# Kernel tuning notes

Measured on AMD Instinct MI355X. Metric: run time of the kernel, lower is better.

The kernel has to match this reference:

```python
import jax, jax.numpy as jnp
import numpy as np

D_MODEL = 2048
N_HEADS = 32
N_KV = 8
HEAD_DIM = D_MODEL // N_HEADS  # 64
D_FF = 8192
ROPE_BASE = 10000.0
EPS = 1e-5
B, S = 2, 2048


def setup_inputs() -> dict:
    key = jax.random.key(0)
    ks = jax.random.split(key, 8)
    s = 0.02
    qkv_out = (N_HEADS + 2 * N_KV) * HEAD_DIM
    return {
        "x": jax.random.normal(ks[0], (B, S, D_MODEL), jnp.float32),
        "w_norm1": jnp.ones((D_MODEL,), jnp.float32),
        "w_qkv": jax.random.normal(ks[1], (D_MODEL, qkv_out), jnp.float32) * s,
        "w_out": jax.random.normal(ks[2], (D_MODEL, D_MODEL), jnp.float32) * s,
        "w_norm2": jnp.ones((D_MODEL,), jnp.float32),
        "w_gate": jax.random.normal(ks[3], (D_MODEL, D_FF), jnp.float32) * s,
        "w_up": jax.random.normal(ks[4], (D_MODEL, D_FF), jnp.float32) * s,
        "w_down": jax.random.normal(ks[5], (D_FF, D_MODEL), jnp.float32) * s,
    }


def _rmsnorm(x, w):
    var = jnp.mean(x * x, axis=-1, keepdims=True)
    return x * jax.lax.rsqrt(var + EPS) * w


def _rope(x, cos, sin):
    # x: [b, s, h, d]; cos/sin: [s, d/2]; non-interleaved (NeoX half split)
    half = x.shape[-1] // 2
    x1, x2 = x[..., :half], x[..., half:]
    c = cos[None, :, None, :]
    sn = sin[None, :, None, :]
    return jnp.concatenate([x1 * c - x2 * sn, x1 * sn + x2 * c], axis=-1)


def _forward(x, w_norm1, w_qkv, w_out, w_norm2, w_gate, w_up, w_down):
    b, s, d = x.shape
    # --- attention block ---
    h = _rmsnorm(x, w_norm1)
    qkv = h @ w_qkv  # [b, s, (H + 2*KV) * hd]
    q = qkv[..., : N_HEADS * HEAD_DIM].reshape(b, s, N_HEADS, HEAD_DIM)
    kv = qkv[..., N_HEADS * HEAD_DIM:].reshape(b, s, 2, N_KV, HEAD_DIM)
    k, v = kv[:, :, 0], kv[:, :, 1]

    inv_freq = 1.0 / (ROPE_BASE ** (jnp.arange(0, HEAD_DIM, 2, dtype=jnp.float32) / HEAD_DIM))
    t = jnp.arange(s, dtype=jnp.float32)
    freqs = t[:, None] * inv_freq[None, :]  # [s, hd/2]
    cos, sin = jnp.cos(freqs), jnp.sin(freqs)
    q = _rope(q, cos, sin)
    k = _rope(k, cos, sin)

    # GQA: repeat_interleave kv heads to match q heads
    g = N_HEADS // N_KV
    k = jnp.repeat(k, g, axis=2)  # [b, s, H, hd]
    v = jnp.repeat(v, g, axis=2)

    scale = 1.0 / np.sqrt(HEAD_DIM)
    scores = jnp.einsum("bqhd,bkhd->bhqk", q, k) * scale
    causal = jnp.tril(jnp.ones((s, s), bool))
    scores = jnp.where(causal[None, None], scores, jnp.finfo(scores.dtype).min)
    attn = jax.nn.softmax(scores, axis=-1)
    ctx = jnp.einsum("bhqk,bkhd->bqhd", attn, v).reshape(b, s, N_HEADS * HEAD_DIM)
    x = x + ctx @ w_out

    # --- MLP block (SwiGLU) ---
    h2 = _rmsnorm(x, w_norm2)
    mlp = (jax.nn.silu(h2 @ w_gate) * (h2 @ w_up)) @ w_down
    return x + mlp


def reference(x, w_norm1, w_qkv, w_out, w_norm2, w_gate, w_up, w_down):
    return _forward(x, w_norm1, w_qkv, w_out, w_norm2, w_gate, w_up, w_down)
```

## Files before the change

kernel.cpp:

```cpp
#include <hip/hip_runtime.h>
#include <stdint.h>

#define D_MODEL 2048
#define S_LEN   2048
#define NTOK    4096
#define QKV_N   3072
#define DFF     8192

typedef float  f32x4   __attribute__((ext_vector_type(4)));
typedef float  f32x16  __attribute__((ext_vector_type(16)));
typedef __bf16 bf16x8  __attribute__((ext_vector_type(8)));
typedef unsigned short u16;
typedef unsigned short u16x8 __attribute__((ext_vector_type(8)));

__device__ __forceinline__ float b2f(u16 u){ union{float f; uint32_t i;} v; v.i = ((uint32_t)u) << 16; return v.f; }
__device__ __forceinline__ u16 f2b(float f){
  union{float f; uint32_t i;} v; v.f = f;
  uint32_t r = v.i + 0x7FFFu + ((v.i >> 16) & 1u);
  return (u16)(r >> 16);
}

__device__ __forceinline__ void gload_lds16(const void* gsrc, void* ldst){
  __builtin_amdgcn_global_load_lds(
      (const __attribute__((address_space(1))) void*)gsrc,
      (__attribute__((address_space(3))) void*)ldst,
      16, 0, 0);
}

__global__ __launch_bounds__(256) void wconv_kernel(const float* __restrict__ W, u16* __restrict__ WT,
                                                    int Nfull, int Kt, int Nt, int k0g, int n0g)
{
  __shared__ float tile[64][65];
  const int nTn = Nt >> 6;
  const int tk = blockIdx.x / nTn, tn = blockIdx.x % nTn;
  const int k0 = tk << 6, n0 = tn << 6;
  const int t  = threadIdx.x;
  const int c4 = (t & 15) << 2;
  const int r  = t >> 4;
#pragma unroll
  for (int i = 0; i < 4; ++i) {
    float4 v = *reinterpret_cast<const float4*>(&W[(size_t)(k0g + k0 + r + i*16) * Nfull + n0g + n0 + c4]);
    tile[r + i*16][c4+0] = v.x; tile[r + i*16][c4+1] = v.y;
    tile[r + i*16][c4+2] = v.z; tile[r + i*16][c4+3] = v.w;
  }
  __syncthreads();
#pragma unroll
  for (int i = 0; i < 4; ++i) {
    int n = r + i*16;
    ushort4 ov;
    ov.x = f2b(tile[c4+0][n]); ov.y = f2b(tile[c4+1][n]);
    ov.z = f2b(tile[c4+2][n]); ov.w = f2b(tile[c4+3][n]);
    *reinterpret_cast<ushort4*>(&WT[(size_t)(n0 + n) * Kt + k0 + c4]) = ov;
  }
}

__global__ void sincos_kernel(float* __restrict__ ct, float* __restrict__ st)
{
  int idx = blockIdx.x * 256 + threadIdx.x;
  if (idx >= S_LEN * 32) return;
  int p = idx >> 5, i = idx & 31;
  double freq = pow(10000.0, -((double)(2*i)) / 64.0);
  double ang  = (double)p * freq;
  ct[idx] = (float)cos(ang);
  st[idx] = (float)sin(ang);
}

template<bool BF16IN>
__global__ __launch_bounds__(256) void rmsnorm_kernel(const void* __restrict__ xin, const float* __restrict__ w, u16* __restrict__ out)
{
  const int row = blockIdx.x;
  const int t = threadIdx.x;
  float v[8];
  if (BF16IN) {
    const u16* xr = ((const u16*)xin) + (size_t)row * D_MODEL;
    u16x8 a = *reinterpret_cast<const u16x8*>(&xr[t*8]);
#pragma unroll
    for (int j = 0; j < 8; ++j) v[j] = b2f(a[j]);
  } else {
    const float* xr = ((const float*)xin) + (size_t)row * D_MODEL;
    float4 a = *reinterpret_cast<const float4*>(&xr[t*8]);
    float4 c = *reinterpret_cast<const float4*>(&xr[t*8+4]);
    v[0]=a.x; v[1]=a.y; v[2]=a.z; v[3]=a.w; v[4]=c.x; v[5]=c.y; v[6]=c.z; v[7]=c.w;
  }
  float ss = 0.f;
#pragma unroll
  for (int j = 0; j < 8; ++j) ss += v[j]*v[j];
#pragma unroll
  for (int d = 1; d < 64; d <<= 1) ss += __shfl_xor(ss, d);
  __shared__ float red[4];
  if ((t & 63) == 0) red[t >> 6] = ss;
  __syncthreads();
  ss = red[0] + red[1] + red[2] + red[3];
  const float sc = rsqrtf(ss * (1.0f / (float)D_MODEL) + 1e-5f);
  float4 w0 = *reinterpret_cast<const float4*>(&w[t*8]);
  float4 w1 = *reinterpret_cast<const float4*>(&w[t*8+4]);
  u16x8 o;
  o[0]=f2b(v[0]*sc*w0.x); o[1]=f2b(v[1]*sc*w0.y); o[2]=f2b(v[2]*sc*w0.z); o[3]=f2b(v[3]*sc*w0.w);
  o[4]=f2b(v[4]*sc*w1.x); o[5]=f2b(v[5]*sc*w1.y); o[6]=f2b(v[6]*sc*w1.z); o[7]=f2b(v[7]*sc*w1.w);
  *reinterpret_cast<u16x8*>(&out[(size_t)row * D_MODEL + t*8]) = o;
}

template<int EPI>
__device__ __forceinline__ void epi_store(size_t idx, float v, float* Cf, u16* Cb,
                                          const float* resf, const u16* resb, const u16* other)
{
  if (EPI == 2)      Cb[idx] = f2b(v / (1.0f + __expf(-v)));
  else if (EPI == 3) Cb[idx] = f2b(v * b2f(other[idx]));
  else if (EPI == 4) Cb[idx] = f2b(v);
  else if (EPI == 5) Cf[idx] += v;
  else if (EPI == 6) Cb[idx] = f2b(v + resf[idx]);
  else if (EPI == 7) Cf[idx] = v + b2f(resb[idx]);
}

template<int EPI>
__global__ __launch_bounds__(512, 2) void gemm8p_kernel(
    const u16* __restrict__ A, const u16* __restrict__ BT,
    int K, int lda, int ldb, int ldc, int n_off,
    float* Cf, u16* Cb,
    const float* __restrict__ resf, const u16* __restrict__ resb, const u16* other)
{
  __shared__ u16 lds[65536];
  const int tid = threadIdx.x;
  const int w = tid >> 6, lane = tid & 63;
  const int g = lane >> 4, lr = lane & 15;
  const int wm = w >> 2, wn = w & 3;
  const int bn = blockIdx.x, bm = blockIdx.y;
  const int NT = K >> 6;
  const int NI = NT >> 1;

  const int srow = tid >> 3;
  const int sg   = (tid & 7) ^ (srow & 7);
  const u16* Asrc = A  + (size_t)(bm * 256) * lda;
  const u16* Bsrc = BT + (size_t)(bn * 256) * ldb;

  const int agc0 = ((0 + g) ^ (lr & 7)) * 8;
  const int agc1 = ((4 + g) ^ (lr & 7)) * 8;

  f32x4 acc[8][4];
#pragma unroll
  for (int i = 0; i < 8; ++i)
#pragma unroll
    for (int j = 0; j < 4; ++j) acc[i][j] = (f32x4){0.f, 0.f, 0.f, 0.f};
  bf16x8 af[4][2], bf0[2][2], bf1[2][2];

#define STAGE_H(isB, h, b, T) do {                                           \
    int tc = ((T) < NT) ? (T) : (NT - 1);                                    \
    const u16* sb = (isB) ? Bsrc : Asrc;                                     \
    const int  sld = (isB) ? ldb : lda;                                      \
    const u16* s0 = sb + (size_t)((h)*128 + srow) * sld + tc*64 + sg*8;      \
    u16* dst = &lds[(b)*32768 + (isB)*16384 + (h)*8192 + tid*8];             \
    gload_lds16(s0, dst);                                                    \
    gload_lds16(s0 + (size_t)64 * sld, dst + 4096);                          \
  } while (0)

#define LOADA(mih, b) { _Pragma("unroll") for (int q = 0; q < 4; ++q) {      \
    const u16* rp = &lds[(b)*32768 + (wm*128 + (mih)*64 + q*16 + lr) * 64];  \
    af[q][0] = *(const bf16x8*)(rp + agc0);                                  \
    af[q][1] = *(const bf16x8*)(rp + agc1); } }

#define LOADB(dst, nih, b) { _Pragma("unroll") for (int nq = 0; nq < 2; ++nq) { \
    const u16* rp = &lds[(b)*32768 + 16384 + (wn*64 + (nih)*32 + nq*16 + lr) * 64]; \
    dst[nq][0] = *(const bf16x8*)(rp + agc0);                                \
    dst[nq][1] = *(const bf16x8*)(rp + agc1); } }

#define MM(mih, nih, BF) {                                                   \
    __builtin_amdgcn_s_setprio(1);                                           \
    _Pragma("unroll") for (int kk = 0; kk < 2; ++kk)                         \
      _Pragma("unroll") for (int q = 0; q < 4; ++q)                          \
        _Pragma("unroll") for (int nq = 0; nq < 2; ++nq)                     \
          acc[(mih)*4+q][(nih)*2+nq] = __builtin_amdgcn_mfma_f32_16x16x32_bf16( \
              af[q][kk], BF[nq][kk], acc[(mih)*4+q][(nih)*2+nq], 0, 0, 0);   \
    __builtin_amdgcn_s_setprio(0); }

#define SYNC_MID  __builtin_amdgcn_s_barrier();                              \
                  asm volatile("s_waitcnt lgkmcnt(0)" ::: "memory");         \
                  __builtin_amdgcn_sched_barrier(0);
#define PHEND     __builtin_amdgcn_s_barrier();
#define PHEND_VM  asm volatile("s_waitcnt vmcnt(4)" ::: "memory");           \
                  __builtin_amdgcn_s_barrier();

  STAGE_H(0, 0, 0, 0); STAGE_H(0, 1, 0, 0);
  STAGE_H(1, 0, 0, 0); STAGE_H(1, 1, 0, 0);
  STAGE_H(1, 0, 1, 1); STAGE_H(1, 1, 1, 1);
  asm volatile("s_waitcnt vmcnt(4)" ::: "memory");
  __builtin_amdgcn_s_barrier();

  for (int i = 0; i < NI; ++i) {
    const int t0 = 2 * i;
    LOADA(0, 0); LOADB(bf0, 0, 0);
    STAGE_H(0, 0, 1, t0 + 1);
    SYNC_MID; MM(0, 0, bf0); PHEND;
    LOADB(bf1, 1, 0);
    STAGE_H(0, 1, 1, t0 + 1);
    SYNC_MID; MM(0, 1, bf1); PHEND;
    LOADA(1, 0);
    STAGE_H(1, 0, 0, t0 + 2);
    SYNC_MID; MM(1, 1, bf1); PHEND;
    STAGE_H(1, 1, 0, t0 + 2);
    SYNC_MID; MM(1, 0, bf0); PHEND_VM;
    LOADA(0, 1); LOADB(bf0, 0, 1);
    STAGE_H(0, 0, 0, t0 + 2);
    SYNC_MID; MM(0, 0, bf0); PHEND;
    LOADB(bf1, 1, 1);
    STAGE_H(0, 1, 0, t0 + 2);
    SYNC_MID; MM(0, 1, bf1); PHEND;
    LOADA(1, 1);
    STAGE_H(1, 0, 1, t0 + 3);
    SYNC_MID; MM(1, 1, bf1); PHEND;
    STAGE_H(1, 1, 1, t0 + 3);
    SYNC_MID; MM(1, 0, bf0); PHEND_VM;
  }
#undef STAGE_H
#undef LOADA
#undef LOADB
#undef MM

#pragma unroll
  for (int mi = 0; mi < 8; ++mi) {
    const int rowOff = (mi >> 2) * 64 + (mi & 3) * 16;
#pragma unroll
    for (int ni = 0; ni < 4; ++ni) {
      const int colOff = (ni >> 1) * 32 + (ni & 1) * 16;
#pragma unroll
      for (int j = 0; j < 4; ++j) {
        int row = bm*256 + wm*128 + rowOff + g*4 + j;
        int col = n_off + bn*256 + wn*64 + colOff + lr;
        epi_store<EPI>((size_t)row * ldc + col, acc[mi][ni][j], Cf, Cb, resf, resb, other);
      }
    }
  }
}

template<int EPI>
__global__ __launch_bounds__(512) void gemm128_kernel(
    const u16* __restrict__ A, const u16* __restrict__ BT,
    int K, int lda, int ldb, int ldc, int n_off,
    float* Cf, u16* Cb,
    const float* __restrict__ resf, const u16* __restrict__ resb, const u16* other)
{
  __shared__ u16 lds[49152];
  const int tid = threadIdx.x;
  const int w = tid >> 6, lane = tid & 63;
  const int g = lane >> 4, lr = lane & 15;
  const int wm = w >> 2, wn = w & 3;
  const int bn = blockIdx.x, bm = blockIdx.y;
  const int NT = K >> 6;
  const int NI = NT >> 1;

  const int srow = tid >> 3;
  const int sg   = (tid & 7) ^ (srow & 7);
  const u16* Asrc = A  + (size_t)(bm * 128) * lda;
  const u16* Bsrc = BT + (size_t)(bn * 256) * ldb;

  const int agc0 = ((0 + g) ^ (lr & 7)) * 8;
  const int agc1 = ((4 + g) ^ (lr & 7)) * 8;

  f32x4 acc[4][4];
#pragma unroll
  for (int i = 0; i < 4; ++i)
#pragma unroll
    for (int j = 0; j < 4; ++j) acc[i][j] = (f32x4){0.f, 0.f, 0.f, 0.f};
  bf16x8 af[2][2], bf0[2][2], bf1[2][2];

#define STAGE_A(b, T) do {                                                   \
    int tc = ((T) < NT) ? (T) : (NT - 1);                                    \
    const u16* s0 = Asrc + (size_t)srow * lda + tc*64 + sg*8;                \
    u16* dst = &lds[(b)*24576 + tid*8];                                      \
    gload_lds16(s0, dst);                                                    \
    gload_lds16(s0 + (size_t)64 * lda, dst + 4096);                          \
  } while (0)

#define STAGE_BH(h, b, T) do {                                               \
    int tc = ((T) < NT) ? (T) : (NT - 1);                                    \
    const u16* s0 = Bsrc + (size_t)((h)*128 + srow) * ldb + tc*64 + sg*8;    \
    u16* dst = &lds[(b)*24576 + 8192 + (h)*8192 + tid*8];                    \
    gload_lds16(s0, dst);                                                    \
    gload_lds16(s0 + (size_t)64 * ldb, dst + 4096);                         \
  } while (0)

#define LOADA(mih, b) { _Pragma("unroll") for (int q = 0; q < 2; ++q) {      \
    const u16* rp = &lds[(b)*24576 + (wm*64 + (mih)*32 + q*16 + lr) * 64];   \
    af[q][0] = *(const bf16x8*)(rp + agc0);                                  \
    af[q][1] = *(const bf16x8*)(rp + agc1); } }

#define LOADB(dst, nih, b) { _Pragma("unroll") for (int nq = 0; nq < 2; ++nq) { \
    const u16* rp = &lds[(b)*24576 + 8192 + (wn*64 + (nih)*32 + nq*16 + lr) * 64]; \
    dst[nq][0] = *(const bf16x8*)(rp + agc0);                                \
    dst[nq][1] = *(const bf16x8*)(rp + agc1); } }

#define MM(mih, nih, BF) {                                                   \
    __builtin_amdgcn_s_setprio(1);                                           \
    _Pragma("unroll") for (int kk = 0; kk < 2; ++kk)                         \
      _Pragma("unroll") for (int q = 0; q < 2; ++q)                          \
        _Pragma("unroll") for (int nq = 0; nq < 2; ++nq)                     \
          acc[(mih)*2+q][(nih)*2+nq] = __builtin_amdgcn_mfma_f32_16x16x32_bf16( \
              af[q][kk], BF[nq][kk], acc[(mih)*2+q][(nih)*2+nq], 0, 0, 0);   \
    __builtin_amdgcn_s_setprio(0); }

  STAGE_A(0, 0); STAGE_BH(0, 0, 0); STAGE_BH(1, 0, 0);
  STAGE_BH(0, 1, 1); STAGE_BH(1, 1, 1);
  asm volatile("s_waitcnt vmcnt(4)" ::: "memory");
  __builtin_amdgcn_s_barrier();

  for (int i = 0; i < NI; ++i) {
    const int t0 = 2 * i;
    LOADA(0, 0); LOADB(bf0, 0, 0);
    STAGE_A(1, t0 + 1);
    SYNC_MID; MM(0, 0, bf0); PHEND;
    LOADB(bf1, 1, 0);
    STAGE_BH(0, 0, t0 + 2);
    SYNC_MID; MM(0, 1, bf1); PHEND;
    LOADA(1, 0);
    STAGE_BH(1, 0, t0 + 2);
    SYNC_MID; MM(1, 1, bf1); PHEND;
    STAGE_A(0, t0 + 2);
    SYNC_MID; MM(1, 0, bf0);
    asm volatile("s_waitcnt vmcnt(6)" ::: "memory");
    __builtin_amdgcn_s_barrier();
    LOADA(0, 1); LOADB(bf0, 0, 1);
    SYNC_MID; MM(0, 0, bf0); PHEND;
    LOADB(bf1, 1, 1);
    STAGE_BH(0, 1, t0 + 3);
    SYNC_MID; MM(0, 1, bf1); PHEND;
    LOADA(1, 1);
    STAGE_BH(1, 1, t0 + 3);
    SYNC_MID; MM(1, 1, bf1); PHEND;
    SYNC_MID; MM(1, 0, bf0);
    asm volatile("s_waitcnt vmcnt(4)" ::: "memory");
    __builtin_amdgcn_s_barrier();
  }
#undef STAGE_A
#undef STAGE_BH
#undef LOADA
#undef LOADB
#undef MM
#undef SYNC_MID
#undef PHEND
#undef PHEND_VM

#pragma unroll
  for (int mi = 0; mi < 4; ++mi) {
    const int rowOff = (mi >> 1) * 32 + (mi & 1) * 16;
#pragma unroll
    for (int ni = 0; ni < 4; ++ni) {
      const int colOff = (ni >> 1) * 32 + (ni & 1) * 16;
#pragma unroll
      for (int j = 0; j < 4; ++j) {
        int row = bm*128 + wm*64 + rowOff + g*4 + j;
        int col = n_off + bn*256 + wn*64 + colOff + lr;
        epi_store<EPI>((size_t)row * ldc + col, acc[mi][ni][j], Cf, Cb, resf, resb, other);
      }
    }
  }
}

__global__ __launch_bounds__(256) void rope_kernel(
    const u16* __restrict__ qkv, const float* __restrict__ ct, const float* __restrict__ st,
    u16* __restrict__ Q, u16* __restrict__ Kt, u16* __restrict__ VT)
{
  const int tok = blockIdx.x;
  const int b = tok >> 11, s = tok & (S_LEN - 1);
  const int w = threadIdx.x >> 6, lane = threadIdx.x & 63;
  const size_t base = (size_t)tok * QKV_N;
  for (int slot = w; slot < 48; slot += 4) {
    int col = (slot < 32) ? slot * 64 : (slot < 40 ? 2048 + (slot - 32) * 64 : 2560 + (slot - 40) * 64);
    float v = b2f(qkv[base + col + lane]);
    if (slot < 40) {
      int i = lane & 31;
      float c = ct[s * 32 + i], sn = st[s * 32 + i];
      float p = b2f(qkv[base + col + (lane ^ 32)]);
      v = (lane < 32) ? (v * c - p * sn) : (v * c + p * sn);
    }
    u16 ob = f2b(v);
    if (slot < 32)      Q [((size_t)(b * 32 + slot)      * S_LEN + s) * 64 + lane] = ob;
    else if (slot < 40) Kt[((size_t)(b * 8 + slot - 32)  * S_LEN + s) * 64 + lane] = ob;
    else                VT[((size_t)(b * 8 + slot - 40)  * 64 + lane) * S_LEN + s] = ob;
  }
}

#define ASCALE 0.1803368801111204f
__global__ __launch_bounds__(256, 3) void attn_kernel(
    const u16* __restrict__ Q, const u16* __restrict__ Kt,
    const u16* __restrict__ VT, u16* __restrict__ ctx)
{
  const int bh  = blockIdx.x;
  const int qb  = 15 - blockIdx.y;
  const int wid = threadIdx.x >> 6;
  const int lane = threadIdx.x & 63;
  const int b = bh >> 5, h = bh & 31;
  const int kvh = (b << 3) + (h >> 2);
  const int q0 = qb * 128 + wid * 32;
  const int cq = lane & 31;
  const int hi = lane >> 5;

  const u16* Qb = Q  + ((size_t)bh * S_LEN + q0) * 64;
  const u16* Kp = Kt + (size_t)kvh * S_LEN * 64 + cq * 64 + hi * 8;
  const u16* Vbase = VT + (size_t)kvh * 64 * S_LEN + hi * 8;
  const u16* Vp[4];
#pragma unroll
  for (int v = 0; v < 4; ++v)
    Vp[v] = Vbase + (size_t)((v & 1) * 32 + cq) * S_LEN + (v >> 1) * 16;

  bf16x8 qf[4];
#pragma unroll
  for (int t = 0; t < 4; ++t)
    qf[t] = *reinterpret_cast<const bf16x8*>(&Qb[cq * 64 + t * 16 + hi * 8]);

  f32x16 o0 = {}, o1 = {};
  float m = -1e30f, l = 0.f;

  __shared__ float xch[4][32];

  const int nt = qb * 4 + wid + 1;

#define ATT_LOADK(KF, T) { _Pragma("unroll") for (int q_ = 0; q_ < 4; ++q_) \
    KF[q_] = *(const bf16x8*)(Kp + (T) * 2048 + q_ * 16); }
#define ATT_LOADV(VF, T) { _Pragma("unroll") for (int v_ = 0; v_ < 4; ++v_) \
    VF[v_] = *(const bf16x8*)(Vp[v_] + (T) * 32); }

#define ATT_COMPUTE(KF, VF, T) do {                                          \
    f32x16 sA = {}, sB = {};                                                 \
    sA = __builtin_amdgcn_mfma_f32_32x32x16_bf16(KF[0], qf[0], sA, 0, 0, 0); \
    sB = __builtin_amdgcn_mfma_f32_32x32x16_bf16(KF[1], qf[1], sB, 0, 0, 0); \
    sA = __builtin_amdgcn_mfma_f32_32x32x16_bf16(KF[2], qf[2], sA, 0, 0, 0); \
    sB = __builtin_amdgcn_mfma_f32_32x32x16_bf16(KF[3], qf[3], sB, 0, 0, 0); \
    float p[16];                                                             \
    _Pragma("unroll") for (int r = 0; r < 16; ++r) p[r] = (sA[r] + sB[r]) * ASCALE; \
    if ((T) == nt - 1) {                                                     \
      _Pragma("unroll") for (int r = 0; r < 16; ++r) {                       \
        int kk = (r & 3) + 8 * (r >> 2) + 4 * hi;                            \
        if (kk > cq) p[r] = -1e30f;                                          \
      }                                                                      \
    }                                                                        \
    float m0_ = fmaxf(fmaxf(p[0], p[1]), p[2]);                              \
    float m1_ = fmaxf(fmaxf(p[3], p[4]), p[5]);                              \
    float m2_ = fmaxf(fmaxf(p[6], p[7]), p[8]);                              \
    float m3_ = fmaxf(fmaxf(p[9], p[10]), p[11]);                            \
    float m4_ = fmaxf(fmaxf(p[12], p[13]), p[14]);                           \
    float tmax = fmaxf(fmaxf(fmaxf(m0_, m1_), m2_), fmaxf(fmaxf(m3_, m4_), p[15])); \
    tmax = fmaxf(tmax, __shfl_xor(tmax, 32));                                \
    if (!__all(tmax <= m + 8.0f)) {                                          \
      float mn = fmaxf(m, tmax);                                             \
      float corr = exp2f(m - mn);                                            \
      m = mn;                                                                \
      l *= corr;                                                             \
      if (hi == 0) xch[wid][cq] = corr;                                      \
      asm volatile("s_waitcnt lgkmcnt(0)" ::: "memory");                     \
      __builtin_amdgcn_sched_barrier(0);                                     \
      float4 c0 = *reinterpret_cast<const float4*>(&xch[wid][4 * hi + 0]);   \
      float4 c1 = *reinterpret_cast<const float4*>(&xch[wid][4 * hi + 8]);   \
      float4 c2 = *reinterpret_cast<const float4*>(&xch[wid][4 * hi + 16]);  \
      float4 c3 = *reinterpret_cast<const float4*>(&xch[wid][4 * hi + 24]);  \
      float ca[16] = {c0.x,c0.y,c0.z,c0.w, c1.x,c1.y,c1.z,c1.w,              \
                      c2.x,c2.y,c2.z,c2.w, c3.x,c3.y,c3.z,c3.w};             \
      _Pragma("unroll") for (int r = 0; r < 16; ++r) { o0[r] *= ca[r]; o1[r] *= ca[r]; } \
    }                                                                        \
    float tsum = 0.f;                                                        \
    _Pragma("unroll") for (int r = 0; r < 16; ++r) { p[r] = exp2f(p[r] - m); tsum += p[r]; } \
    l += tsum;                                                               \
    uint32_t wds[8], pw[8];                                                  \
    _Pragma("unroll") for (int j = 0; j < 8; ++j) {                          \
      uint32_t wv;                                                           \
      asm("v_cvt_pk_bf16_f32 %0, %1, %2" : "=v"(wv) : "v"(p[2*j]), "v"(p[2*j+1])); \
      wds[j] = wv;                                                           \
    }                                                                        \
    _Pragma("unroll") for (int j = 0; j < 8; ++j) pw[j] = __shfl_xor(wds[j], 32); \
    union { uint32_t u[4]; bf16x8 v; } pa0, pa1;                             \
    pa0.u[0] = hi ? pw[2]  : wds[0];                                         \
    pa0.u[1] = hi ? pw[3]  : wds[1];                                         \
    pa0.u[2] = hi ? wds[2] : pw[0];                                          \
    pa0.u[3] = hi ? wds[3] : pw[1];                                          \
    pa1.u[0] = hi ? pw[6]  : wds[4];                                         \
    pa1.u[1] = hi ? pw[7]  : wds[5];                                         \
    pa1.u[2] = hi ? wds[6] : pw[4];                                          \
    pa1.u[3] = hi ? wds[7] : pw[5];                                          \
    o0 = __builtin_amdgcn_mfma_f32_32x32x16_bf16(pa0.v, VF[0], o0, 0, 0, 0); \
    o0 = __builtin_amdgcn_mfma_f32_32x32x16_bf16(pa1.v, VF[2], o0, 0, 0, 0); \
    o1 = __builtin_amdgcn_mfma_f32_32x32x16_bf16(pa0.v, VF[1], o1, 0, 0, 0); \
    o1 = __builtin_amdgcn_mfma_f32_32x32x16_bf16(pa1.v, VF[3], o1, 0, 0, 0); \
  } while (0)

  bf16x8 kf0[4], kf1[4], vf[4];
  ATT_LOADK(kf0, 0);
  for (int t = 0; t < nt; ) {
    if (t + 1 < nt) ATT_LOADK(kf1, t + 1);
    ATT_LOADV(vf, t);
    ATT_COMPUTE(kf0, vf, t);
    ++t; if (t >= nt) break;
    if (t + 1 < nt) ATT_LOADK(kf0, t + 1);
    ATT_LOADV(vf, t);
    ATT_COMPUTE(kf1, vf, t);
    ++t;
  }
#undef ATT_LOADK
#undef ATT_LOADV
#undef ATT_COMPUTE

  l += __shfl_xor(l, 32);
  float linv = 1.0f / l;
  if (hi == 0) xch[wid][cq] = linv;
  asm volatile("s_waitcnt lgkmcnt(0)" ::: "memory");
  __builtin_amdgcn_sched_barrier(0);
  float4 n0 = *reinterpret_cast<const float4*>(&xch[wid][4 * hi + 0]);
  float4 n1 = *reinterpret_cast<const float4*>(&xch[wid][4 * hi + 8]);
  float4 n2 = *reinterpret_cast<const float4*>(&xch[wid][4 * hi + 16]);
  float4 n3 = *reinterpret_cast<const float4*>(&xch[wid][4 * hi + 24]);
  float na[16] = {n0.x,n0.y,n0.z,n0.w, n1.x,n1.y,n1.z,n1.w,
                  n2.x,n2.y,n2.z,n2.w, n3.x,n3.y,n3.z,n3.w};
#pragma unroll
  for (int r = 0; r < 16; ++r) {
    int row = (r & 3) + 8 * (r >> 2) + 4 * hi;
    size_t base = (size_t)(b * S_LEN + q0 + row) * D_MODEL + h * 64;
    ctx[base + cq]      = f2b(o0[r] * na[r]);
    ctx[base + 32 + cq] = f2b(o1[r] * na[r]);
  }
}

extern "C" void kernel_launch(void* const* d_in, const int* in_sizes, int n_in,
                              void* d_out, int out_size, void* d_ws, size_t ws_size,
                              hipStream_t stream)
{
  const float* x     = (const float*)d_in[0];
  const float* wn1   = (const float*)d_in[1];
  const float* wqkv  = (const float*)d_in[2];
  const float* wout  = (const float*)d_in[3];
  const float* wn2   = (const float*)d_in[4];
  const float* wgate = (const float*)d_in[5];
  const float* wup   = (const float*)d_in[6];
  const float* wdown = (const float*)d_in[7];
  float* out = (float*)d_out;
  char* ws = (char*)d_ws;

  float* cosT = (float*)(ws + 0);
  float* sinT = (float*)(ws + 262144);
  u16*   wT   = (u16*)  (ws + 524288);
  u16*   hB   = (u16*)  (ws + 17301504);
  u16*   x1b  = (u16*)  (ws + 34078720);
  char*  S    = ws + 50855936;
  u16*   qkvB = (u16*)(S + 0);
  u16*   qB   = (u16*)(S + 25165824);
  u16*   kB   = (u16*)(S + 41943040);
  u16*   vtB  = (u16*)(S + 46137344);
  u16*   ctxB = (u16*)(S + 50331648);
  u16*   gsB  = (u16*)(S + 0);

  sincos_kernel<<<dim3(256), 256, 0, stream>>>(cosT, sinT);
  rmsnorm_kernel<false><<<dim3(NTOK), 256, 0, stream>>>(x, wn1, hB);

  wconv_kernel<<<dim3((2048/64)*(3072/64)), 256, 0, stream>>>(wqkv, wT, 3072, 2048, 3072, 0, 0);
  gemm128_kernel<4><<<dim3(QKV_N/256, NTOK/128), 512, 0, stream>>>(hB, wT, 2048, 2048, 2048, 3072, 0, nullptr, qkvB, nullptr, nullptr, nullptr);
  rope_kernel<<<dim3(NTOK), 256, 0, stream>>>(qkvB, cosT, sinT, qB, kB, vtB);
  attn_kernel<<<dim3(64, 16), 256, 0, stream>>>(qB, kB, vtB, ctxB);

  wconv_kernel<<<dim3((2048/64)*(2048/64)), 256, 0, stream>>>(wout, wT, 2048, 2048, 2048, 0, 0);
  gemm128_kernel<6><<<dim3(D_MODEL/256, NTOK/128), 512, 0, stream>>>(ctxB, wT, 2048, 2048, 2048, 2048, 0, nullptr, x1b, x, nullptr, nullptr);

  rmsnorm_kernel<true><<<dim3(NTOK), 256, 0, stream>>>(x1b, wn2, hB);

  for (int c = 0; c < 2; ++c) {
    wconv_kernel<<<dim3((2048/64)*(4096/64)), 256, 0, stream>>>(wgate, wT, 8192, 2048, 4096, 0, c*4096);
    gemm8p_kernel<2><<<dim3(4096/256, NTOK/256), 512, 0, stream>>>(hB, wT, 2048, 2048, 2048, 8192, c*4096, nullptr, gsB, nullptr, nullptr, nullptr);
  }
  for (int c = 0; c < 2; ++c) {
    wconv_kernel<<<dim3((2048/64)*(4096/64)), 256, 0, stream>>>(wup, wT, 8192, 2048, 4096, 0, c*4096);
    gemm8p_kernel<3><<<dim3(4096/256, NTOK/256), 512, 0, stream>>>(hB, wT, 2048, 2048, 2048, 8192, c*4096, nullptr, gsB, nullptr, nullptr, gsB);
  }
  wconv_kernel<<<dim3((4096/64)*(2048/64)), 256, 0, stream>>>(wdown, wT, 2048, 4096, 2048, 0, 0);
  gemm128_kernel<7><<<dim3(D_MODEL/256, NTOK/128), 512, 0, stream>>>(gsB, wT, 4096, 8192, 4096, 2048, 0, out, nullptr, nullptr, x1b, nullptr);
  wconv_kernel<<<dim3((4096/64)*(2048/64)), 256, 0, stream>>>(wdown, wT, 2048, 4096, 2048, 4096, 0);
  gemm128_kernel<5><<<dim3(D_MODEL/256, NTOK/128), 512, 0, stream>>>(gsB + 4096, wT, 4096, 8192, 4096, 2048, 0, out, nullptr, nullptr, nullptr, nullptr);
}
```

Baseline: 811.8 us.

## Fuse weight conversion into tails of preceding kernels and restructure MLP chunking

Eliminates most standalone weight transpose/convert launches by appending the conversion of the next GEMM's weights to the tail of preceding kernels (GEMMs, rmsnorm, attention), using double-buffered weight slots. RoPE for Q is moved into the attention kernel, removing the Q write/read round trip. The MLP is restructured into two DFF halves so down-projection runs per half with a narrower intermediate slab. Conversion work now runs serially after each kernel's main work in the same blocks, which may lengthen those kernels and relies on correct slot reuse ordering.

```diff
diff --git a/kernel.cpp b/kernel.cpp
--- a/kernel.cpp
+++ b/kernel.cpp
@@ -27,31 +27,49 @@
       16, 0, 0);
 }
 
+__device__ __forceinline__ void conv_tiles(const float* W, u16* WT,
+    int Nfull, int Kt, int Nt, int k0g, int n0g, void* ldsbuf)
+{
+  if (W == nullptr) return;
+  float* tf = (float*)ldsbuf;
+  const int tt  = threadIdx.x;
+  const int nTn = Nt >> 6;
+  const int nT  = (Kt >> 6) * nTn;
+  const int bid = blockIdx.y * gridDim.x + blockIdx.x;
+  const int gsz = gridDim.x * gridDim.y;
+  const int c4 = (tt & 15) << 2;
+  const int r  = tt >> 4;
+  for (int tile = bid; tile < nT; tile += gsz) {
+    const int k0 = (tile / nTn) << 6, n0 = (tile % nTn) << 6;
+    __syncthreads();
+    if (tt < 256) {
+#pragma unroll
+      for (int i = 0; i < 4; ++i) {
+        int row = r + i * 16;
+        float4 v = *reinterpret_cast<const float4*>(&W[(size_t)(k0g + k0 + row) * Nfull + n0g + n0 + c4]);
+        tf[row * 65 + c4 + 0] = v.x; tf[row * 65 + c4 + 1] = v.y;
+        tf[row * 65 + c4 + 2] = v.z; tf[row * 65 + c4 + 3] = v.w;
+      }
+    }
+    __syncthreads();
+    if (tt < 256) {
+#pragma unroll
+      for (int i = 0; i < 4; ++i) {
+        int n = r + i * 16;
+        ushort4 ov;
+        ov.x = f2b(tf[(c4 + 0) * 65 + n]); ov.y = f2b(tf[(c4 + 1) * 65 + n]);
+        ov.z = f2b(tf[(c4 + 2) * 65 + n]); ov.w = f2b(tf[(c4 + 3) * 65 + n]);
+        *reinterpret_cast<ushort4*>(&WT[(size_t)(n0 + n) * Kt + k0 + c4]) = ov;
+      }
+    }
+  }
+}
+
 __global__ __launch_bounds__(256) void wconv_kernel(const float* __restrict__ W, u16* __restrict__ WT,
                                                     int Nfull, int Kt, int Nt, int k0g, int n0g)
 {
-  __shared__ float tile[64][65];
-  const int nTn = Nt >> 6;
-  const int tk = blockIdx.x / nTn, tn = blockIdx.x % nTn;
-  const int k0 = tk << 6, n0 = tn << 6;
-  const int t  = threadIdx.x;
-  const int c4 = (t & 15) << 2;
-  const int r  = t >> 4;
-#pragma unroll
-  for (int i = 0; i < 4; ++i) {
-    float4 v = *reinterpret_cast<const float4*>(&W[(size_t)(k0g + k0 + r + i*16) * Nfull + n0g + n0 + c4]);
-    tile[r + i*16][c4+0] = v.x; tile[r + i*16][c4+1] = v.y;
-    tile[r + i*16][c4+2] = v.z; tile[r + i*16][c4+3] = v.w;
-  }
-  __syncthreads();
-#pragma unroll
-  for (int i = 0; i < 4; ++i) {
-    int n = r + i*16;
-    ushort4 ov;
-    ov.x = f2b(tile[c4+0][n]); ov.y = f2b(tile[c4+1][n]);
-    ov.z = f2b(tile[c4+2][n]); ov.w = f2b(tile[c4+3][n]);
-    *reinterpret_cast<ushort4*>(&WT[(size_t)(n0 + n) * Kt + k0 + c4]) = ov;
-  }
+  __shared__ float tile[64 * 65];
+  conv_tiles(W, WT, Nfull, Kt, Nt, k0g, n0g, tile);
 }
 
 __global__ void sincos_kernel(float* __restrict__ ct, float* __restrict__ st)
@@ -66,8 +84,10 @@
 }
 
 template<bool BF16IN>
-__global__ __launch_bounds__(256) void rmsnorm_kernel(const void* __restrict__ xin, const float* __restrict__ w, u16* __restrict__ out)
-{
+__global__ __launch_bounds__(256) void rmsnorm_kernel(const void* __restrict__ xin, const float* __restrict__ w, u16* __restrict__ out,
+                                                      const float* cvW, u16* cvWT, int cvNfull, int cvKt, int cvNt, int cvK0g, int cvN0g)
+{
+  __shared__ float tfbuf[64 * 65];
   const int row = blockIdx.x;
   const int t = threadIdx.x;
   float v[8];
@@ -98,6 +118,7 @@
   o[0]=f2b(v[0]*sc*w0.x); o[1]=f2b(v[1]*sc*w0.y); o[2]=f2b(v[2]*sc*w0.z); o[3]=f2b(v[3]*sc*w0.w);
   o[4]=f2b(v[4]*sc*w1.x); o[5]=f2b(v[5]*sc*w1.y); o[6]=f2b(v[6]*sc*w1.z); o[7]=f2b(v[7]*sc*w1.w);
   *reinterpret_cast<u16x8*>(&out[(size_t)row * D_MODEL + t*8]) = o;
+  conv_tiles(cvW, cvWT, cvNfull, cvKt, cvNt, cvK0g, cvN0g, tfbuf);
 }
 
 template<int EPI>
@@ -117,7 +138,8 @@
     const u16* __restrict__ A, const u16* __restrict__ BT,
     int K, int lda, int ldb, int ldc, int n_off,
     float* Cf, u16* Cb,
-    const float* __restrict__ resf, const u16* __restrict__ resb, const u16* other)
+    const float* __restrict__ resf, const u16* __restrict__ resb, const u16* other,
+    const float* cvW, u16* cvWT, int cvNfull, int cvKt, int cvNt, int cvK0g, int cvN0g)
 {
   __shared__ u16 lds[65536];
   const int tid = threadIdx.x;
@@ -229,6 +251,7 @@
       }
     }
   }
+  conv_tiles(cvW, cvWT, cvNfull, cvKt, cvNt, cvK0g, cvN0g, lds);
 }
 
 template<int EPI>
@@ -236,7 +259,8 @@
     const u16* __restrict__ A, const u16* __restrict__ BT,
     int K, int lda, int ldb, int ldc, int n_off,
     float* Cf, u16* Cb,
-    const float* __restrict__ resf, const u16* __restrict__ resb, const u16* other)
+    const float* __restrict__ resf, const u16* __restrict__ resb, const u16* other,
+    const float* cvW, u16* cvWT, int cvNfull, int cvKt, int cvNt, int cvK0g, int cvN0g)
 {
   __shared__ u16 lds[49152];
   const int tid = threadIdx.x;
@@ -352,37 +376,40 @@
       }
     }
   }
+  conv_tiles(cvW, cvWT, cvNfull, cvKt, cvNt, cvK0g, cvN0g, lds);
 }
 
 __global__ __launch_bounds__(256) void rope_kernel(
     const u16* __restrict__ qkv, const float* __restrict__ ct, const float* __restrict__ st,
-    u16* __restrict__ Q, u16* __restrict__ Kt, u16* __restrict__ VT)
+    u16* __restrict__ Kt, u16* __restrict__ VT)
 {
   const int tok = blockIdx.x;
   const int b = tok >> 11, s = tok & (S_LEN - 1);
   const int w = threadIdx.x >> 6, lane = threadIdx.x & 63;
   const size_t base = (size_t)tok * QKV_N;
-  for (int slot = w; slot < 48; slot += 4) {
-    int col = (slot < 32) ? slot * 64 : (slot < 40 ? 2048 + (slot - 32) * 64 : 2560 + (slot - 40) * 64);
+  for (int slot = w; slot < 16; slot += 4) {
+    int col = (slot < 8) ? 2048 + slot * 64 : 2560 + (slot - 8) * 64;
     float v = b2f(qkv[base + col + lane]);
-    if (slot < 40) {
+    if (slot < 8) {
       int i = lane & 31;
       float c = ct[s * 32 + i], sn = st[s * 32 + i];
       float p = b2f(qkv[base + col + (lane ^ 32)]);
       v = (lane < 32) ? (v * c - p * sn) : (v * c + p * sn);
     }
     u16 ob = f2b(v);
-    if (slot < 32)      Q [((size_t)(b * 32 + slot)      * S_LEN + s) * 64 + lane] = ob;
-    else if (slot < 40) Kt[((size_t)(b * 8 + slot - 32)  * S_LEN + s) * 64 + lane] = ob;
-    else                VT[((size_t)(b * 8 + slot - 40)  * 64 + lane) * S_LEN + s] = ob;
+    if (slot < 8) Kt[((size_t)(b * 8 + slot)     * S_LEN + s) * 64 + lane] = ob;
+    else          VT[((size_t)(b * 8 + slot - 8) * 64 + lane) * S_LEN + s] = ob;
   }
 }
 
 #define ASCALE 0.1803368801111204f
 __global__ __launch_bounds__(256, 3) void attn_kernel(
-    const u16* __restrict__ Q, const u16* __restrict__ Kt,
-    const u16* __restrict__ VT, u16* __restrict__ ctx)
-{
+    const u16* __restrict__ qkv, const u16* __restrict__ Kt,
+    const u16* __restrict__ VT, u16* __restrict__ ctx,
+    const float* __restrict__ ct, const float* __restrict__ st,
+    const float* cvW, u16* cvWT, int cvNfull, int cvKt, int cvNt, int cvK0g, int cvN0g)
+{
+  __shared__ float tfbuf[64 * 65];
   const int bh  = blockIdx.x;
   const int qb  = 15 - blockIdx.y;
   const int wid = threadIdx.x >> 6;
@@ -393,7 +420,6 @@
   const int cq = lane & 31;
   const int hi = lane >> 5;
 
-  const u16* Qb = Q  + ((size_t)bh * S_LEN + q0) * 64;
   const u16* Kp = Kt + (size_t)kvh * S_LEN * 64 + cq * 64 + hi * 8;
   const u16* Vbase = VT + (size_t)kvh * 64 * S_LEN + hi * 8;
   const u16* Vp[4];
@@ -402,9 +428,33 @@
     Vp[v] = Vbase + (size_t)((v & 1) * 32 + cq) * S_LEN + (v >> 1) * 16;
 
   bf16x8 qf[4];
-#pragma unroll
-  for (int t = 0; t < 4; ++t)
-    qf[t] = *reinterpret_cast<const bf16x8*>(&Qb[cq * 64 + t * 16 + hi * 8]);
+  {
+    const u16* Qr = qkv + (size_t)(b * S_LEN + q0 + cq) * QKV_N + h * 64 + hi * 8;
+    u16 qr[4][8];
+#pragma unroll
+    for (int t = 0; t < 4; ++t)
+      *reinterpret_cast<u16x8*>(qr[t]) = *reinterpret_cast<const u16x8*>(Qr + t * 16);
+    const float* cb = ct + (size_t)(q0 + cq) * 32 + hi * 8;
+    const float* sb = st + (size_t)(q0 + cq) * 32 + hi * 8;
+    union { u16 u[8]; bf16x8 v; } qo[4];
+#pragma unroll
+    for (int t = 0; t < 2; ++t) {
+      float4 c0 = *reinterpret_cast<const float4*>(cb + 16 * t);
+      float4 c1 = *reinterpret_cast<const float4*>(cb + 16 * t + 4);
+      float4 s0 = *reinterpret_cast<const float4*>(sb + 16 * t);
+      float4 s1 = *reinterpret_cast<const float4*>(sb + 16 * t + 4);
+      float cc[8] = {c0.x,c0.y,c0.z,c0.w, c1.x,c1.y,c1.z,c1.w};
+      float ssn[8] = {s0.x,s0.y,s0.z,s0.w, s1.x,s1.y,s1.z,s1.w};
+#pragma unroll
+      for (int i = 0; i < 8; ++i) {
+        float lo = b2f(qr[t][i]), hif = b2f(qr[t + 2][i]);
+        qo[t].u[i]     = f2b(lo * cc[i] - hif * ssn[i]);
+        qo[t + 2].u[i] = f2b(hif * cc[i] + lo * ssn[i]);
+      }
+    }
+#pragma unroll
+    for (int t = 0; t < 4; ++t) qf[t] = qo[t].v;
+  }
 
   f32x16 o0 = {}, o1 = {};
   float m = -1e30f, l = 0.f;
@@ -514,8 +564,10 @@
     ctx[base + cq]      = f2b(o0[r] * na[r]);
     ctx[base + 32 + cq] = f2b(o1[r] * na[r]);
   }
-}
-
+  conv_tiles(cvW, cvWT, cvNfull, cvKt, cvNt, cvK0g, cvN0g, tfbuf);
+}
+
+#define NOCV nullptr, nullptr, 0, 0, 0, 0, 0
 extern "C" void kernel_launch(void* const* d_in, const int* in_sizes, int n_in,
                               void* d_out, int out_size, void* d_ws, size_t ws_size,
                               hipStream_t stream)
@@ -531,42 +583,46 @@
   float* out = (float*)d_out;
   char* ws = (char*)d_ws;
 
-  float* cosT = (float*)(ws + 0);
-  float* sinT = (float*)(ws + 262144);
-  u16*   wT   = (u16*)  (ws + 524288);
-  u16*   hB   = (u16*)  (ws + 17301504);
-  u16*   x1b  = (u16*)  (ws + 34078720);
-  char*  S    = ws + 50855936;
-  u16*   qkvB = (u16*)(S + 0);
-  u16*   qB   = (u16*)(S + 25165824);
-  u16*   kB   = (u16*)(S + 41943040);
-  u16*   vtB  = (u16*)(S + 46137344);
-  u16*   ctxB = (u16*)(S + 50331648);
-  u16*   gsB  = (u16*)(S + 0);
+  float* cosT  = (float*)(ws + 0);
+  float* sinT  = (float*)(ws + 262144);
+  u16*   slotA = (u16*)  (ws + 524288);
+  u16*   slotB = (u16*)  (ws + 17301504);
+  u16*   x1b   = (u16*)  (ws + 34078720);
+  char*  S     = ws + 50855936;
+  u16*   hB    = (u16*)(S + 0);
+  u16*   qkvB  = (u16*)(S + 16777216);
+  u16*   kB    = (u16*)(S + 41943040);
+  u16*   vtB   = (u16*)(S + 46137344);
+  u16*   ctxB  = (u16*)(S + 0);
+  u16*   h2B   = (u16*)(S + 0);
+  u16*   slab  = (u16*)(S + 16777216);
 
   sincos_kernel<<<dim3(256), 256, 0, stream>>>(cosT, sinT);
-  rmsnorm_kernel<false><<<dim3(NTOK), 256, 0, stream>>>(x, wn1, hB);
-
-  wconv_kernel<<<dim3((2048/64)*(3072/64)), 256, 0, stream>>>(wqkv, wT, 3072, 2048, 3072, 0, 0);
-  gemm128_kernel<4><<<dim3(QKV_N/256, NTOK/128), 512, 0, stream>>>(hB, wT, 2048, 2048, 2048, 3072, 0, nullptr, qkvB, nullptr, nullptr, nullptr);
-  rope_kernel<<<dim3(NTOK), 256, 0, stream>>>(qkvB, cosT, sinT, qB, kB, vtB);
-  attn_kernel<<<dim3(64, 16), 256, 0, stream>>>(qB, kB, vtB, ctxB);
-
-  wconv_kernel<<<dim3((2048/64)*(2048/64)), 256, 0, stream>>>(wout, wT, 2048, 2048, 2048, 0, 0);
-  gemm128_kernel<6><<<dim3(D_MODEL/256, NTOK/128), 512, 0, stream>>>(ctxB, wT, 2048, 2048, 2048, 2048, 0, nullptr, x1b, x, nullptr, nullptr);
-
-  rmsnorm_kernel<true><<<dim3(NTOK), 256, 0, stream>>>(x1b, wn2, hB);
-
-  for (int c = 0; c < 2; ++c) {
-    wconv_kernel<<<dim3((2048/64)*(4096/64)), 256, 0, stream>>>(wgate, wT, 8192, 2048, 4096, 0, c*4096);
-    gemm8p_kernel<2><<<dim3(4096/256, NTOK/256), 512, 0, stream>>>(hB, wT, 2048, 2048, 2048, 8192, c*4096, nullptr, gsB, nullptr, nullptr, nullptr);
-  }
-  for (int c = 0; c < 2; ++c) {
-    wconv_kernel<<<dim3((2048/64)*(4096/64)), 256, 0, stream>>>(wup, wT, 8192, 2048, 4096, 0, c*4096);
-    gemm8p_kernel<3><<<dim3(4096/256, NTOK/256), 512, 0, stream>>>(hB, wT, 2048, 2048, 2048, 8192, c*4096, nullptr, gsB, nullptr, nullptr, gsB);
-  }
-  wconv_kernel<<<dim3((4096/64)*(2048/64)), 256, 0, stream>>>(wdown, wT, 2048, 4096, 2048, 0, 0);
-  gemm128_kernel<7><<<dim3(D_MODEL/256, NTOK/128), 512, 0, stream>>>(gsB, wT, 4096, 8192, 4096, 2048, 0, out, nullptr, nullptr, x1b, nullptr);
-  wconv_kernel<<<dim3((4096/64)*(2048/64)), 256, 0, stream>>>(wdown, wT, 2048, 4096, 2048, 4096, 0);
-  gemm128_kernel<5><<<dim3(D_MODEL/256, NTOK/128), 512, 0, stream>>>(gsB + 4096, wT, 4096, 8192, 4096, 2048, 0, out, nullptr, nullptr, nullptr, nullptr);
-}
+  rmsnorm_kernel<false><<<dim3(NTOK), 256, 0, stream>>>(x, wn1, hB, NOCV);
+  wconv_kernel<<<dim3(1536), 256, 0, stream>>>(wqkv, slotA, 3072, 2048, 3072, 0, 0);
+
+  gemm128_kernel<4><<<dim3(12, 32), 512, 0, stream>>>(hB, slotA, 2048, 2048, 2048, 3072, 0,
+      nullptr, qkvB, nullptr, nullptr, nullptr, wout, slotB, 2048, 2048, 2048, 0, 0);
+  rope_kernel<<<dim3(NTOK), 256, 0, stream>>>(qkvB, cosT, sinT, kB, vtB);
+  attn_kernel<<<dim3(64, 16), 256, 0, stream>>>(qkvB, kB, vtB, ctxB, cosT, sinT,
+      wgate, slotA, 8192, 2048, 4096, 0, 0);
+
+  gemm128_kernel<6><<<dim3(8, 32), 512, 0, stream>>>(ctxB, slotB, 2048, 2048, 2048, 2048, 0,
+      nullptr, x1b, x, nullptr, nullptr, NOCV);
+
+  rmsnorm_kernel<true><<<dim3(NTOK), 256, 0, stream>>>(x1b, wn2, h2B,
+      wup, slotB, 8192, 2048, 4096, 0, 0);
+
+  gemm8p_kernel<2><<<dim3(16, 16), 512, 0, stream>>>(h2B, slotA, 2048, 2048, 2048, 4096, 0,
+      nullptr, slab, nullptr, nullptr, nullptr, NOCV);
+  gemm8p_kernel<3><<<dim3(16, 16), 512, 0, stream>>>(h2B, slotB, 2048, 2048, 2048, 4096, 0,
+      nullptr, slab, nullptr, nullptr, slab, wdown, slotA, 2048, 4096, 2048, 0, 0);
+  gemm128_kernel<7><<<dim3(8, 32), 512, 0, stream>>>(slab, slotA, 4096, 4096, 4096, 2048, 0,
+      out, nullptr, nullptr, x1b, nullptr, wgate, slotB, 8192, 2048, 4096, 0, 4096);
+  gemm8p_kernel<2><<<dim3(16, 16), 512, 0, stream>>>(h2B, slotB, 2048, 2048, 2048, 4096, 0,
+      nullptr, slab, nullptr, nullptr, nullptr, wup, slotA, 8192, 2048, 4096, 0, 4096);
+  gemm8p_kernel<3><<<dim3(16, 16), 512, 0, stream>>>(h2B, slotA, 2048, 2048, 2048, 4096, 0,
+      nullptr, slab, nullptr, nullptr, slab, wdown, slotB, 2048, 4096, 2048, 4096, 0);
+  gemm128_kernel<5><<<dim3(8, 32), 512, 0, stream>>>(slab, slotB, 4096, 4096, 4096, 2048, 0,
+      out, nullptr, nullptr, nullptr, nullptr, NOCV);
+}
```

Result: faster. 791.4 us (-2.5%).
